# Kernel tuning notes

Measured on AMD Instinct MI355X. Metric: run time of the kernel, lower is better.

The kernel has to match this reference:

```python
import jax, jax.numpy as jnp
import numpy as np

DIM = 384
WS = 7
N = WS * WS
H = 12
HD = DIM // H
SCALE = HD ** -0.5
B_ = 4096
NW = 64


def _rel_pos_index():
    ii, jj = np.meshgrid(np.arange(WS), np.arange(WS), indexing='ij')
    flat = np.stack([ii.ravel(), jj.ravel()])  # [2, N]
    rel = flat[:, :, None] - flat[:, None, :]  # [2, N, N]
    rel = rel.transpose(1, 2, 0)
    rel[:, :, 0] += WS - 1
    rel[:, :, 1] += WS - 1
    rel[:, :, 0] *= 2 * WS - 1
    return jnp.asarray(rel.sum(-1), dtype=jnp.int32)  # [N, N]


def setup_inputs() -> dict:
    key = jax.random.key(0)
    ks = jax.random.split(key, 7)
    return {
        'x': jax.random.normal(ks[0], (B_, N, DIM), dtype=jnp.float32),
        'mask': jax.random.normal(ks[1], (NW, N, N), dtype=jnp.float32),
        'qkv_w': jax.random.normal(ks[2], (3 * DIM, DIM), dtype=jnp.float32) * 0.02,
        'qkv_b': jax.random.normal(ks[3], (3 * DIM,), dtype=jnp.float32) * 0.02,
        'proj_w': jax.random.normal(ks[4], (DIM, DIM), dtype=jnp.float32) * 0.02,
        'proj_b': jax.random.normal(ks[5], (DIM,), dtype=jnp.float32) * 0.02,
        'rel_bias_table': jax.random.normal(ks[6], ((2 * WS - 1) ** 2, H), dtype=jnp.float32) * 0.02,
        'rel_pos_index': _rel_pos_index(),
    }


def reference(x, mask, qkv_w, qkv_b, proj_w, proj_b, rel_bias_table, rel_pos_index):
    b_, n, c = x.shape
    h, hd = H, c // H
    qkv = x @ qkv_w.T + qkv_b  # [B_, N, 3C]
    qkv = qkv.reshape(b_, n, 3, h, hd)
    q, k, v = qkv[:, :, 0], qkv[:, :, 1], qkv[:, :, 2]  # [B_, N, H, hd]
    attn = jnp.einsum('bnhd,bmhd->bhnm', q, k) * SCALE  # [B_, H, N, N]
    bias = rel_bias_table[rel_pos_index]  # [N, N, H]
    attn = attn + jnp.transpose(bias, (2, 0, 1))[None]
    nw = mask.shape[0]
    attn = attn.reshape(b_ // nw, nw, h, n, n) + mask[None, :, None]
    attn = attn.reshape(b_, h, n, n)
    attn = jax.nn.softmax(attn, axis=-1)
    out = jnp.einsum('bhnm,bmhd->bnhd', attn, v).reshape(b_, n, c)
    return out @ proj_w.T + proj_b
```

## Files before the change

### kernel.cpp

```cpp
#include <hip/hip_runtime.h>
#include <hip/hip_bf16.h>

typedef __attribute__((ext_vector_type(4))) float  f32x4;
typedef __attribute__((ext_vector_type(8))) short  s16x8;

#define DEVI static __device__ __forceinline__

constexpr int   BQ    = 4096;
constexpr int   NTOK  = 49;
constexpr int   DIMC  = 384;
constexpr int   NH    = 12;
constexpr int   HDIM  = 32;
constexpr int   NW    = 64;
constexpr int   QKVN  = 3 * DIMC;
constexpr float SCALE_ = 0.17677669529663687f;

DEVI ushort f2bf(float f) {
  union { float f; unsigned u; } v; v.f = f;
  unsigned r = v.u + 0x7fffu + ((v.u >> 16) & 1u);
  return (ushort)(r >> 16);
}

DEVI void async_ld16(const ushort* g, const ushort* l) {
  auto gp = reinterpret_cast<const __attribute__((address_space(1))) unsigned int*>(
      reinterpret_cast<uintptr_t>(g));
  auto lp = reinterpret_cast<__attribute__((address_space(3))) unsigned int*>(
      reinterpret_cast<uintptr_t>(l));
  __builtin_amdgcn_global_load_lds(gp, lp, 16, 0, 0);
}

__global__ void cast_x_kernel(const float* __restrict__ x, ushort* __restrict__ o, int n8) {
  int i = blockIdx.x * 256 + threadIdx.x;
  const int stride = gridDim.x * 256;
  for (; i < n8; i += stride) {
    f32x4 a = *(const f32x4*)(x + (size_t)i * 8);
    f32x4 b = *(const f32x4*)(x + (size_t)i * 8 + 4);
    s16x8 v;
    v[0] = (short)f2bf(a[0]); v[1] = (short)f2bf(a[1]);
    v[2] = (short)f2bf(a[2]); v[3] = (short)f2bf(a[3]);
    v[4] = (short)f2bf(b[0]); v[5] = (short)f2bf(b[1]);
    v[6] = (short)f2bf(b[2]); v[7] = (short)f2bf(b[3]);
    *(s16x8*)(o + (size_t)i * 8) = v;
  }
}

constexpr int PREP_N1 = QKVN * DIMC;
constexpr int PREP_N2 = DIMC * DIMC;
constexpr int PREP_N3 = NW * NH * 16 * 64;
constexpr int PREP_N4 = QKVN;
__global__ void prep_kernel(const float* __restrict__ qkv_w, const float* __restrict__ proj_w,
                            const float* __restrict__ tab, const int* __restrict__ idx,
                            const float* __restrict__ mask, const float* __restrict__ qkv_b,
                            ushort* __restrict__ qw, ushort* __restrict__ pw,
                            float* __restrict__ combP, float* __restrict__ qbias) {
  int i = blockIdx.x * 256 + threadIdx.x;
  if (i < PREP_N1) {
    int n = i / DIMC;
    float sc = (n < DIMC) ? SCALE_ : 1.0f;
    qw[i] = f2bf(qkv_w[i] * sc);
  } else if (i < PREP_N1 + PREP_N2) {
    int j = i - PREP_N1;
    pw[j] = f2bf(proj_w[j]);
  } else if (i < PREP_N1 + PREP_N2 + PREP_N3) {
    int j = i - PREP_N1 - PREP_N2;
    int lane = j & 63;
    int tile = (j >> 6) & 15;
    int wh   = j >> 10;
    int h = wh % NH, w = wh / NH;
    int it = tile >> 2, jt = tile & 3;
    int c = jt * 16 + (lane & 15);
    f32x4 v;
    #pragma unroll
    for (int r = 0; r < 4; r++) {
      int rr = it * 16 + (lane >> 4) * 4 + r;
      v[r] = (rr < NTOK && c < NTOK)
           ? tab[idx[rr * NTOK + c] * NH + h] + mask[(size_t)w * NTOK * NTOK + rr * NTOK + c]
           : -1.0e30f;
    }
    ((f32x4*)combP)[j] = v;
  } else if (i < PREP_N1 + PREP_N2 + PREP_N3 + PREP_N4) {
    int j = i - PREP_N1 - PREP_N2 - PREP_N3;
    qbias[j] = qkv_b[j] * ((j < DIMC) ? SCALE_ : 1.0f);
  }
}

template<int EPI, int K, int NB>
__global__ __launch_bounds__(256) void gemm_bt_kernel(
    const ushort* __restrict__ Ap, const ushort* __restrict__ Bp,
    const float* __restrict__ bias, float* __restrict__ outF,
    ushort* __restrict__ outBF)
{
  struct MB { ushort A[2][128 * 32]; ushort B[2][128 * 32]; };
  union ShU { MB mb; ushort Ct[128 * 136]; };
  __shared__ ShU sh;

  const int tid  = threadIdx.x;
  const int lane = tid & 63;
  const int wv   = tid >> 6;
  const int wm   = (wv >> 1) * 64, wn = (wv & 1) * 64;
  const int l15  = lane & 15, lg = lane >> 4;
  constexpr int NT = NB * 128;

  const int chunk = gridDim.x >> 3;
  const int wgid  = (blockIdx.x & 7) * chunk + (blockIdx.x >> 3);
  const int nbase = (wgid % NB) * 128;
  const int mbase = (wgid / NB) * 128;

  const int srow = lane >> 2;
  const int scol = (lane & 3) * 8;

  const ushort* Abase = Ap + (size_t)(mbase + wv * 32 + srow) * K + scol;
  const ushort* Bbase = Bp + (size_t)(nbase + wv * 32 + srow) * K + scol;

  f32x4 acc[4][4];
  #pragma unroll
  for (int i = 0; i < 4; i++)
    #pragma unroll
    for (int j = 0; j < 4; j++) acc[i][j] = (f32x4){0.f, 0.f, 0.f, 0.f};

  auto stage = [&](int buf, int k0) {
    #pragma unroll
    for (int i = 0; i < 2; i++) {
      async_ld16(Abase + (size_t)i * 16 * K + k0, &sh.mb.A[buf][(wv * 32 + i * 16) * 32]);
      async_ld16(Bbase + (size_t)i * 16 * K + k0, &sh.mb.B[buf][(wv * 32 + i * 16) * 32]);
    }
  };
  auto compute = [&](int buf) {
    s16x8 af[4], bfv[4];
    #pragma unroll
    for (int t = 0; t < 4; t++) af[t]  = *(const s16x8*)&sh.mb.A[buf][(wm + t*16 + l15) * 32 + lg*8];
    #pragma unroll
    for (int t = 0; t < 4; t++) bfv[t] = *(const s16x8*)&sh.mb.B[buf][(wn + t*16 + l15) * 32 + lg*8];
    #pragma unroll
    for (int mt = 0; mt < 4; mt++)
      #pragma unroll
      for (int nt = 0; nt < 4; nt++)
        acc[mt][nt] = __builtin_amdgcn_mfma_f32_16x16x32_bf16(af[mt], bfv[nt], acc[mt][nt], 0, 0, 0);
  };

  constexpr int NSTEP = K / 32;
  stage(0, 0);
  __syncthreads();
  #pragma unroll
  for (int t = 1; t < NSTEP; t++) {
    stage(t & 1, t * 32);
    compute((t - 1) & 1);
    __syncthreads();
  }
  compute((NSTEP - 1) & 1);

  if (EPI == 0) {
    #pragma unroll
    for (int mt = 0; mt < 4; mt++)
      #pragma unroll
      for (int nt = 0; nt < 4; nt++) {
        int n = nbase + wn + nt*16 + l15;
        float bv = bias[n];
        #pragma unroll
        for (int r = 0; r < 4; r++) {
          int m = mbase + wm + mt*16 + lg*4 + r;
          outF[(size_t)m * NT + n] = acc[mt][nt][r] + bv;
        }
      }
  } else {
    __syncthreads();
    float bv[4];
    #pragma unroll
    for (int nt = 0; nt < 4; nt++) bv[nt] = bias[nbase + wn + nt*16 + l15];
    #pragma unroll
    for (int mt = 0; mt < 4; mt++)
      #pragma unroll
      for (int nt = 0; nt < 4; nt++) {
        int col = wn + nt*16 + l15;
        #pragma unroll
        for (int r = 0; r < 4; r++)
          sh.Ct[(wm + mt*16 + lg*4 + r) * 136 + col] = f2bf(acc[mt][nt][r] + bv[nt]);
      }
    __syncthreads();
    #pragma unroll
    for (int i = 0; i < 8; i++) {
      int c = tid + i * 256;
      int row = c >> 4, col8 = (c & 15) * 8;
      *(s16x8*)(outBF + (size_t)(mbase + row) * NT + nbase + col8) =
          *(const s16x8*)&sh.Ct[row * 136 + col8];
    }
  }
}

__global__ __launch_bounds__(256, 4) void attn_kernel(
    const ushort* __restrict__ QKVb, const float* __restrict__ combP,
    ushort* __restrict__ Ob)
{
  __shared__ ushort PV[4][64][72];
  const int b    = blockIdx.x;
  const int tid  = threadIdx.x;
  const int lane = tid & 63, wv = tid >> 6;
  const int l15  = lane & 15, lg = lane >> 4;
  const int widx = b & (NW - 1);

  for (int hi = 0; hi < 3; hi++) {
    const int h = wv * 3 + hi;
    const ushort* Wq = QKVb + (size_t)b * NTOK * QKVN + h * HDIM;
    const f32x4*  cp = (const f32x4*)combP + ((size_t)widx * NH + h) * (16 * 64) + lane;

    s16x8 qf[4], kf[4];
    #pragma unroll
    for (int t = 0; t < 4; t++) {
      int r = t*16 + l15; r = r > 48 ? 48 : r;
      qf[t] = *(const s16x8*)(Wq + (size_t)r*QKVN + lg*8);
      kf[t] = *(const s16x8*)(Wq + DIMC + (size_t)r*QKVN + lg*8);
    }

    {
      s16x8 vrow[4];
      #pragma unroll
      for (int c = 0; c < 4; c++)
        vrow[c] = (lane < NTOK) ? *(const s16x8*)(Wq + 2*DIMC + (size_t)lane*QKVN + c*8)
                                : (s16x8){0,0,0,0,0,0,0,0};
      #pragma unroll
      for (int c = 0; c < 4; c++)
        #pragma unroll
        for (int e = 0; e < 8; e++)
          PV[wv][c*8 + e][lane] = (ushort)vrow[c][e];
    }

    f32x4 s[4][4];
    #pragma unroll
    for (int it = 0; it < 4; it++)
      #pragma unroll
      for (int jt = 0; jt < 4; jt++) s[it][jt] = (f32x4){0.f,0.f,0.f,0.f};
    #pragma unroll
    for (int it = 0; it < 4; it++)
      #pragma unroll
      for (int jt = 0; jt < 4; jt++)
        s[it][jt] = __builtin_amdgcn_mfma_f32_16x16x32_bf16(qf[it], kf[jt], s[it][jt], 0, 0, 0);

    float rmax[4][4];
    #pragma unroll
    for (int it = 0; it < 4; it++)
      #pragma unroll
      for (int r = 0; r < 4; r++) rmax[it][r] = -3.0e38f;
    #pragma unroll
    for (int it = 0; it < 4; it++)
      #pragma unroll
      for (int jt = 0; jt < 4; jt++) {
        f32x4 cadd = cp[(it*4 + jt) * 64];
        #pragma unroll
        for (int r = 0; r < 4; r++) {
          float v = s[it][jt][r] + cadd[r];
          s[it][jt][r] = v;
          rmax[it][r] = fmaxf(rmax[it][r], v);
        }
      }
    #pragma unroll
    for (int it = 0; it < 4; it++)
      #pragma unroll
      for (int r = 0; r < 4; r++)
        #pragma unroll
        for (int x = 1; x < 16; x <<= 1)
          rmax[it][r] = fmaxf(rmax[it][r], __shfl_xor(rmax[it][r], x));

    float rsum[4][4];
    #pragma unroll
    for (int it = 0; it < 4; it++)
      #pragma unroll
      for (int r = 0; r < 4; r++) rsum[it][r] = 0.f;
    #pragma unroll
    for (int it = 0; it < 4; it++)
      #pragma unroll
      for (int jt = 0; jt < 4; jt++)
        #pragma unroll
        for (int r = 0; r < 4; r++) {
          float e = __expf(s[it][jt][r] - rmax[it][r]);
          s[it][jt][r] = e;
          rsum[it][r] += e;
        }
    #pragma unroll
    for (int it = 0; it < 4; it++)
      #pragma unroll
      for (int r = 0; r < 4; r++)
        #pragma unroll
        for (int x = 1; x < 16; x <<= 1)
          rsum[it][r] += __shfl_xor(rsum[it][r], x);

    s16x8 vf[2][2];
    #pragma unroll
    for (int nt = 0; nt < 2; nt++)
      #pragma unroll
      for (int kk = 0; kk < 2; kk++)
        vf[nt][kk] = *(const s16x8*)&PV[wv][nt*16 + l15][kk*32 + lg*8];
    asm volatile("s_waitcnt lgkmcnt(0)" ::: "memory");
    __builtin_amdgcn_sched_barrier(0);

    #pragma unroll
    for (int it = 0; it < 4; it++)
      #pragma unroll
      for (int jt = 0; jt < 4; jt++)
        #pragma unroll
        for (int r = 0; r < 4; r++)
          PV[wv][it*16 + lg*4 + r][jt*16 + l15] = f2bf(s[it][jt][r]);

    f32x4 o[4][2];
    #pragma unroll
    for (int it = 0; it < 4; it++)
      #pragma unroll
      for (int nt = 0; nt < 2; nt++) o[it][nt] = (f32x4){0.f,0.f,0.f,0.f};
    #pragma unroll
    for (int it = 0; it < 4; it++)
      #pragma unroll
      for (int kk = 0; kk < 2; kk++) {
        s16x8 pf = *(const s16x8*)&PV[wv][it*16 + l15][kk*32 + lg*8];
        #pragma unroll
        for (int nt = 0; nt < 2; nt++)
          o[it][nt] = __builtin_amdgcn_mfma_f32_16x16x32_bf16(pf, vf[nt][kk], o[it][nt], 0, 0, 0);
      }

    #pragma unroll
    for (int it = 0; it < 4; it++)
      #pragma unroll
      for (int r = 0; r < 4; r++) {
        int q = it*16 + lg*4 + r;
        if (q < NTOK) {
          float ri = 1.0f / rsum[it][r];
          #pragma unroll
          for (int nt = 0; nt < 2; nt++)
            Ob[((size_t)b*NTOK + q)*DIMC + h*HDIM + nt*16 + l15] = f2bf(o[it][nt][r] * ri);
        }
      }
  }
}

extern "C" void kernel_launch(void* const* d_in, const int* in_sizes, int n_in,
                              void* d_out, int out_size, void* d_ws, size_t ws_size,
                              hipStream_t stream)
{
  const float* x      = (const float*)d_in[0];
  const float* mask   = (const float*)d_in[1];
  const float* qkv_w  = (const float*)d_in[2];
  const float* qkv_b  = (const float*)d_in[3];
  const float* proj_w = (const float*)d_in[4];
  const float* proj_b = (const float*)d_in[5];
  const float* rtab   = (const float*)d_in[6];
  const int*   ridx   = (const int*)d_in[7];
  float* out = (float*)d_out;

  char* p = (char*)d_ws;
  auto alloc = [&](size_t bytes) { char* r = p; p += (bytes + 255) & ~(size_t)255; return r; };
  ushort* xb    = (ushort*)alloc((size_t)BQ*NTOK*DIMC*2);
  ushort* QKVb  = (ushort*)alloc((size_t)BQ*NTOK*QKVN*2);
  ushort* Ob    = (ushort*)alloc((size_t)BQ*NTOK*DIMC*2);
  ushort* qw    = (ushort*)alloc((size_t)QKVN*DIMC*2);
  ushort* pw    = (ushort*)alloc((size_t)DIMC*DIMC*2);
  float*  cbP   = (float*)alloc((size_t)NW*NH*16*64*4*4);
  float*  qbias = (float*)alloc((size_t)QKVN*4);

  const int n8 = BQ*NTOK*DIMC/8;
  cast_x_kernel<<<2048, 256, 0, stream>>>(x, xb, n8);
  prep_kernel<<<(PREP_N1+PREP_N2+PREP_N3+PREP_N4 + 255)/256, 256, 0, stream>>>(
      qkv_w, proj_w, rtab, ridx, mask, qkv_b, qw, pw, cbP, qbias);

  gemm_bt_kernel<1, DIMC, 9><<<14112, 256, 0, stream>>>(xb, qw, qbias, nullptr, QKVb);

  attn_kernel<<<BQ, 256, 0, stream>>>(QKVb, cbP, Ob);

  gemm_bt_kernel<0, DIMC, 3><<<4704, 256, 0, stream>>>(Ob, pw, proj_b, out, nullptr);
}
```

Baseline: 810.7 us.

## Write QKV head-major from GEMM epilogue and triple-buffer GEMM K-loop

The QKV GEMM epilogue now scatters its bf16 output into separate Q, K and V buffers laid out as [batch, head, token, head_dim], so each attention head reads a contiguous 49x32 block instead of rows strided by 1152 elements. The GEMM main loop moves from double to triple buffering in LDS, with an explicit vmcnt wait and a raw barrier so two tiles are in flight while one is computed. The intent is better coalescing in the attention loads and more latency hiding in the GEMM. In exchange, LDS use per block grows, and the epilogue does an integer divide per store.

Result: no change. 812.6 us (+0.2%).

```diff
diff --git a/kernel.cpp b/kernel.cpp
--- a/kernel.cpp
+++ b/kernel.cpp
@@ -88,9 +88,9 @@
 __global__ __launch_bounds__(256) void gemm_bt_kernel(
     const ushort* __restrict__ Ap, const ushort* __restrict__ Bp,
     const float* __restrict__ bias, float* __restrict__ outF,
-    ushort* __restrict__ outBF)
+    ushort* __restrict__ Qb, ushort* __restrict__ Kb, ushort* __restrict__ Vb)
 {
-  struct MB { ushort A[2][128 * 32]; ushort B[2][128 * 32]; };
+  struct MB { ushort A[3][128 * 32]; ushort B[3][128 * 32]; };
   union ShU { MB mb; ushort Ct[128 * 136]; };
   __shared__ ShU sh;
 
@@ -140,14 +140,16 @@
 
   constexpr int NSTEP = K / 32;
   stage(0, 0);
-  __syncthreads();
+  stage(1, 32);
   #pragma unroll
-  for (int t = 1; t < NSTEP; t++) {
-    stage(t & 1, t * 32);
-    compute((t - 1) & 1);
-    __syncthreads();
-  }
-  compute((NSTEP - 1) & 1);
+  for (int t = 0; t < NSTEP; t++) {
+    if (t + 1 < NSTEP) { asm volatile("s_waitcnt vmcnt(4)" ::: "memory"); }
+    else               { asm volatile("s_waitcnt vmcnt(0)" ::: "memory"); }
+    __builtin_amdgcn_s_barrier();
+    __builtin_amdgcn_sched_barrier(0);
+    compute(t % 3);
+    if (t + 2 < NSTEP) stage((t + 2) % 3, (t + 2) * 32);
+  }
 
   if (EPI == 0) {
     #pragma unroll
@@ -177,18 +179,27 @@
           sh.Ct[(wm + mt*16 + lg*4 + r) * 136 + col] = f2bf(acc[mt][nt][r] + bv[nt]);
       }
     __syncthreads();
+    const int which = nbase / DIMC;
+    const int h0    = (nbase - which * DIMC) >> 5;
+    ushort* obase = (which == 0) ? Qb : (which == 1) ? Kb : Vb;
     #pragma unroll
     for (int i = 0; i < 8; i++) {
-      int c = tid + i * 256;
-      int row = c >> 4, col8 = (c & 15) * 8;
-      *(s16x8*)(outBF + (size_t)(mbase + row) * NT + nbase + col8) =
-          *(const s16x8*)&sh.Ct[row * 136 + col8];
+      int c    = tid + i * 256;
+      int hs   = c >> 9;
+      int j    = c & 511;
+      int rloc = j >> 2;
+      int d0   = (j & 3) * 8;
+      int m = mbase + rloc;
+      int b = m / NTOK, tok = m - b * NTOK;
+      *(s16x8*)(obase + (((size_t)b * NH + h0 + hs) * NTOK + tok) * HDIM + d0) =
+          *(const s16x8*)&sh.Ct[rloc * 136 + hs * 32 + d0];
     }
   }
 }
 
 __global__ __launch_bounds__(256, 4) void attn_kernel(
-    const ushort* __restrict__ QKVb, const float* __restrict__ combP,
+    const ushort* __restrict__ Qb, const ushort* __restrict__ Kb,
+    const ushort* __restrict__ Vb, const float* __restrict__ combP,
     ushort* __restrict__ Ob)
 {
   __shared__ ushort PV[4][64][72];
@@ -200,22 +211,24 @@
 
   for (int hi = 0; hi < 3; hi++) {
     const int h = wv * 3 + hi;
-    const ushort* Wq = QKVb + (size_t)b * NTOK * QKVN + h * HDIM;
+    const ushort* Qh = Qb + ((size_t)b * NH + h) * NTOK * HDIM;
+    const ushort* Kh = Kb + ((size_t)b * NH + h) * NTOK * HDIM;
+    const ushort* Vh = Vb + ((size_t)b * NH + h) * NTOK * HDIM;
     const f32x4*  cp = (const f32x4*)combP + ((size_t)widx * NH + h) * (16 * 64) + lane;
 
     s16x8 qf[4], kf[4];
     #pragma unroll
     for (int t = 0; t < 4; t++) {
       int r = t*16 + l15; r = r > 48 ? 48 : r;
-      qf[t] = *(const s16x8*)(Wq + (size_t)r*QKVN + lg*8);
-      kf[t] = *(const s16x8*)(Wq + DIMC + (size_t)r*QKVN + lg*8);
+      qf[t] = *(const s16x8*)(Qh + r*HDIM + lg*8);
+      kf[t] = *(const s16x8*)(Kh + r*HDIM + lg*8);
     }
 
     {
       s16x8 vrow[4];
       #pragma unroll
       for (int c = 0; c < 4; c++)
-        vrow[c] = (lane < NTOK) ? *(const s16x8*)(Wq + 2*DIMC + (size_t)lane*QKVN + c*8)
+        vrow[c] = (lane < NTOK) ? *(const s16x8*)(Vh + (size_t)lane*HDIM + c*8)
                                 : (s16x8){0,0,0,0,0,0,0,0};
       #pragma unroll
       for (int c = 0; c < 4; c++)
@@ -347,7 +360,9 @@
   char* p = (char*)d_ws;
   auto alloc = [&](size_t bytes) { char* r = p; p += (bytes + 255) & ~(size_t)255; return r; };
   ushort* xb    = (ushort*)alloc((size_t)BQ*NTOK*DIMC*2);
-  ushort* QKVb  = (ushort*)alloc((size_t)BQ*NTOK*QKVN*2);
+  ushort* Qb    = (ushort*)alloc((size_t)BQ*NH*NTOK*HDIM*2);
+  ushort* Kb    = (ushort*)alloc((size_t)BQ*NH*NTOK*HDIM*2);
+  ushort* Vb    = (ushort*)alloc((size_t)BQ*NH*NTOK*HDIM*2);
   ushort* Ob    = (ushort*)alloc((size_t)BQ*NTOK*DIMC*2);
   ushort* qw    = (ushort*)alloc((size_t)QKVN*DIMC*2);
   ushort* pw    = (ushort*)alloc((size_t)DIMC*DIMC*2);
@@ -359,9 +374,9 @@
   prep_kernel<<<(PREP_N1+PREP_N2+PREP_N3+PREP_N4 + 255)/256, 256, 0, stream>>>(
       qkv_w, proj_w, rtab, ridx, mask, qkv_b, qw, pw, cbP, qbias);
 
-  gemm_bt_kernel<1, DIMC, 9><<<14112, 256, 0, stream>>>(xb, qw, qbias, nullptr, QKVb);
-
-  attn_kernel<<<BQ, 256, 0, stream>>>(QKVb, cbP, Ob);
-
-  gemm_bt_kernel<0, DIMC, 3><<<4704, 256, 0, stream>>>(Ob, pw, proj_b, out, nullptr);
-}
+  gemm_bt_kernel<1, DIMC, 9><<<14112, 256, 0, stream>>>(xb, qw, qbias, nullptr, Qb, Kb, Vb);
+
+  attn_kernel<<<BQ, 256, 0, stream>>>(Qb, Kb, Vb, cbP, Ob);
+
+  gemm_bt_kernel<0, DIMC, 3><<<4704, 256, 0, stream>>>(Ob, pw, proj_b, out, nullptr, nullptr, nullptr);
+}
```
